# Performance work log

Measured on AMD Instinct MI355X. Metric: run time of the kernel, lower is better.

## Reference

```python
import jax, jax.numpy as jnp
import numpy as np

B, N, H = 4, 256, 128
EPS_BN = 1e-5     # nn.BatchNorm default eps
EPS_AGG = 1e-20   # NodeFeatureLayer.epsilon


def _linear_params(key, fan_in, shape_w, shape_b):
    kw, kb = jax.random.split(key)
    bound = 1.0 / np.sqrt(fan_in)
    w = jax.random.uniform(kw, shape_w, minval=-bound, maxval=bound, dtype=jnp.float32)
    b = jax.random.uniform(kb, shape_b, minval=-bound, maxval=bound, dtype=jnp.float32)
    return w, b


def setup_inputs() -> dict:
    key = jax.random.key(0)
    ks = jax.random.split(key, 6)
    Ue_w, Ue_b = _linear_params(ks[2], H, (H, H), (H,))
    Ve_w, Ve_b = _linear_params(ks[3], H, (H, H), (H,))
    Un_w, Un_b = _linear_params(ks[4], H, (H, H), (H,))
    Vn_w, Vn_b = _linear_params(ks[5], H, (H, H), (H,))
    return {
        "x": jax.random.normal(ks[0], (B, N, H), dtype=jnp.float32),
        "e": jax.random.normal(ks[1], (B, N, N, H), dtype=jnp.float32),
        "Ue_w": Ue_w, "Ue_b": Ue_b,   # EdgeFeatureLayer.U
        "Ve_w": Ve_w, "Ve_b": Ve_b,   # EdgeFeatureLayer.V
        "Un_w": Un_w, "Un_b": Un_b,   # NodeFeatureLayer.U
        "Vn_w": Vn_w, "Vn_b": Vn_b,   # NodeFeatureLayer.V
        "bn_x_g": jnp.ones((H,), jnp.float32), "bn_x_b": jnp.zeros((H,), jnp.float32),
        "bn_e_g": jnp.ones((H,), jnp.float32), "bn_e_b": jnp.zeros((H,), jnp.float32),
    }


def _bn(t, gamma, beta, axes):
    # BatchNorm with track_running_stats=False: normalize per-channel (last dim)
    # over all other axes using batch statistics (biased variance).
    m = jnp.mean(t, axis=axes, keepdims=True)
    v = jnp.var(t, axis=axes, keepdims=True)
    return (t - m) * jax.lax.rsqrt(v + EPS_BN) * gamma + beta


def reference(x, e, Ue_w, Ue_b, Ve_w, Ve_b, Un_w, Un_b, Vn_w, Vn_b,
              bn_x_g, bn_x_b, bn_e_g, bn_e_b):
    # EdgeFeatureLayer: Ue + Vx_rows + Vx_cols  -> (B,N,N,H)
    Vx = x @ Ve_w.T + Ve_b                       # (B,N,H)
    e_feat = (e @ Ue_w.T + Ue_b
              + Vx[:, :, None, :]                # rows: unsqueeze(2)
              + Vx[:, None, :, :])               # cols: unsqueeze(1)
    gates = jax.nn.sigmoid(e_feat)               # (B,N,N,H)

    # NodeFeatureLayer: Ux + sum_j(gate_ij * Vx_j) / (eps + sum_j gate_ij)
    Vnx = x @ Vn_w.T + Vn_b                      # (B,N,H)
    num = jnp.einsum('bijh,bjh->bih', gates, Vnx)
    den = EPS_AGG + jnp.sum(gates, axis=2)       # (B,N,H)
    x_feat = x @ Un_w.T + Un_b + num / den

    # norm -> (no dropout) -> relu -> residual
    x_new = x + jax.nn.relu(_bn(x_feat, bn_x_g, bn_x_b, (0, 1)))
    e_new = e + jax.nn.relu(_bn(e_feat, bn_e_g, bn_e_b, (0, 1, 2)))
    return (x_new, e_new)
```

## Files before the change

### kernel.cpp

```cpp
#include <hip/hip_runtime.h>
#include <math.h>

typedef short bf16x8 __attribute__((ext_vector_type(8)));
typedef float f32x4 __attribute__((ext_vector_type(4)));

#define BB 4
#define NN 256
#define HH 128
#define ME_ (BB*NN*NN)

#define VX_OFF   0
#define UX_OFF   131072
#define VXN_OFF  262144
#define NUM_OFF  393216
#define DEN_OFF  655360
#define PSUM_OFF 917504
#define PSQ_OFF  1179648
#define XF_OFF   1441792
#define PSR_OFF  1572864
#define PSQR_OFF 1581056
#define PSX_OFF  1589248
#define PSXX_OFF 1597440
#define SCE_OFF  1605632
#define SHE_OFF  1605760
#define SCX_OFF  1605888
#define SHX_OFF  1606016
#define W16_OFF  1606144

__device__ inline short f2bf(float f) {
    unsigned u = __builtin_bit_cast(unsigned, f);
    u += 0x7FFFu + ((u >> 16) & 1u);
    return (short)(u >> 16);
}
__device__ inline float bfbits2f(unsigned hi) {
    return __builtin_bit_cast(float, hi);
}

__global__ __launch_bounds__(256) void k_prep(const float* __restrict__ W,
                                              unsigned short* __restrict__ W16)
{
    int i = blockIdx.x * 256 + threadIdx.x;
    W16[i] = (unsigned short)f2bf(W[i]);
}

__global__ __launch_bounds__(256) void k_linx(
    const float* __restrict__ x,
    const float* __restrict__ Ve_w, const float* __restrict__ Ve_b,
    const float* __restrict__ Vn_w, const float* __restrict__ Vn_b,
    const float* __restrict__ Un_w, const float* __restrict__ Un_b,
    float* ws)
{
    __shared__ float xs[8 * 128];
    int t = threadIdx.x;
    int rowbase = blockIdx.x * 8;

    const float4* xg = (const float4*)(x + (size_t)rowbase * 128);
    ((float4*)xs)[t] = xg[t];
    __syncthreads();

    int h = t & 127, rh = t >> 7;
    float accV[4], accN[4], accU[4];
    float bV = Ve_b[h], bN = Vn_b[h], bU = Un_b[h];
    #pragma unroll
    for (int q = 0; q < 4; ++q) { accV[q] = bV; accN[q] = bN; accU[q] = bU; }

    const float4* wV = (const float4*)(Ve_w + (size_t)h * 128);
    const float4* wN = (const float4*)(Vn_w + (size_t)h * 128);
    const float4* wU = (const float4*)(Un_w + (size_t)h * 128);

    #pragma unroll 4
    for (int k4 = 0; k4 < 32; ++k4) {
        float4 wv = wV[k4], wn = wN[k4], wu = wU[k4];
        #pragma unroll
        for (int q = 0; q < 4; ++q) {
            float4 xv = *(const float4*)&xs[(rh + 2 * q) * 128 + k4 * 4];
            accV[q] += xv.x*wv.x + xv.y*wv.y + xv.z*wv.z + xv.w*wv.w;
            accN[q] += xv.x*wn.x + xv.y*wn.y + xv.z*wn.z + xv.w*wn.w;
            accU[q] += xv.x*wu.x + xv.y*wu.y + xv.z*wu.z + xv.w*wu.w;
        }
    }
    unsigned* VXN = (unsigned*)(ws + VXN_OFF);
    #pragma unroll
    for (int q = 0; q < 4; ++q) {
        size_t idx = (size_t)(rowbase + rh + 2 * q) * 128 + h;
        ws[VX_OFF + idx] = accV[q];
        ws[UX_OFF + idx] = accU[q];
        VXN[idx] = ((unsigned)(unsigned short)f2bf(accV[q]))
                 | ((unsigned)(unsigned short)f2bf(accN[q]) << 16);
    }
}

__device__ inline void load_raw(const float* __restrict__ eb, int row, int g,
                                float4* raw)
{
    const float* rp = eb + (size_t)row * 128 + g * 8;
    #pragma unroll
    for (int kc = 0; kc < 4; ++kc) {
        raw[2*kc]   = *(const float4*)(rp + kc * 32);
        raw[2*kc+1] = *(const float4*)(rp + kc * 32 + 4);
    }
}
__device__ inline void cvt_frag(const float4* raw, bf16x8* afr)
{
    #pragma unroll
    for (int kc = 0; kc < 4; ++kc) {
        float4 f0 = raw[2*kc], f1 = raw[2*kc+1];
        bf16x8 a;
        a[0] = f2bf(f0.x); a[1] = f2bf(f0.y); a[2] = f2bf(f0.z); a[3] = f2bf(f0.w);
        a[4] = f2bf(f1.x); a[5] = f2bf(f1.y); a[6] = f2bf(f1.z); a[7] = f2bf(f1.w);
        afr[kc] = a;
    }
}
__device__ inline bf16x8 ldsW(const short* Wl, int h, int kc, int g, int swz)
{
    return *(const bf16x8*)((const char*)Wl + h * 256 + ((kc * 64 + g * 16) ^ swz));
}

__global__ __launch_bounds__(256) void k_edge_stats(
    const float* __restrict__ e,
    const unsigned short* __restrict__ W16,
    const float* __restrict__ Ue_b,
    float* __restrict__ ws)
{
    __shared__ short Wl[16384];
    __shared__ float red[2048];
    int t   = threadIdx.x;
    int bx  = blockIdx.x;
    int bi  = bx >> 1, jh = bx & 1;
    int b   = bi >> 8;
    int wid = t >> 6, l = t & 63;
    int hsub = l & 15, g = l >> 4;
    int swz = (hsub & 7) << 4;
    int jbase = jh * 128 + wid * 32;

    const unsigned* VXNb = (const unsigned*)(ws + VXN_OFF) + (size_t)b * 32768;
    const float* eb = e + (size_t)bi * 32768;

    float4 raw[8];
    load_raw(eb, jbase + hsub, g, raw);

    float biasv[8];
    #pragma unroll
    for (int ct = 0; ct < 8; ++ct) {
        int h = ct * 16 + hsub;
        biasv[ct] = Ue_b[h] + ws[VX_OFF + (size_t)bi * 128 + h];
    }

    const int4* Wg = (const int4*)W16;
    #pragma unroll
    for (int p = 0; p < 8; ++p) {
        int s = t + 256 * p;
        int r = s >> 4, c = s & 15;
        int addr = r * 256 + ((c * 16) ^ ((r & 7) << 4));
        *(int4*)((char*)Wl + addr) = Wg[s];
    }
    __syncthreads();

    float num[8] = {0,0,0,0,0,0,0,0}, den[8] = {0,0,0,0,0,0,0,0};
    float se[8]  = {0,0,0,0,0,0,0,0}, sq[8]  = {0,0,0,0,0,0,0,0};

    bf16x8 afr[4];

    #pragma unroll
    for (int rt = 0; rt < 2; ++rt) {
        int jb = jbase + rt * 16;
        cvt_frag(raw, afr);
        if (rt == 0) load_raw(eb, jbase + 16 + hsub, g, raw);

        unsigned pkall[32];
        #pragma unroll
        for (int ct = 0; ct < 8; ++ct)
            #pragma unroll
            for (int r = 0; r < 4; ++r)
                pkall[ct * 4 + r] =
                    VXNb[(size_t)(jb + g * 4 + r) * 128 + ct * 16 + hsub];

        #pragma unroll
        for (int ct = 0; ct < 8; ++ct) {
            int h = ct * 16 + hsub;

            f32x4 acc = {0.f, 0.f, 0.f, 0.f};
            #pragma unroll
            for (int kc = 0; kc < 4; ++kc)
                acc = __builtin_amdgcn_mfma_f32_16x16x32_bf16(
                          afr[kc], ldsW(Wl, h, kc, g, swz), acc, 0, 0, 0);

            float bih = biasv[ct];
            #pragma unroll
            for (int r = 0; r < 4; ++r) {
                unsigned pk = pkall[ct * 4 + r];
                float vx  = bfbits2f(pk << 16);
                float vnx = bfbits2f(pk & 0xFFFF0000u);
                float v = acc[r] + bih + vx;
                float gv = __builtin_amdgcn_rcpf(1.0f + __expf(-v));
                num[ct] += gv * vnx;
                den[ct] += gv;
                se[ct]  += v;
                sq[ct]  += v * v;
            }
        }
    }

    #pragma unroll
    for (int ct = 0; ct < 8; ++ct) {
        float n = num[ct], d = den[ct], s1 = se[ct], s2 = sq[ct];
        n  += __shfl_xor(n, 32);  n  += __shfl_xor(n, 16);
        d  += __shfl_xor(d, 32);  d  += __shfl_xor(d, 16);
        s1 += __shfl_xor(s1, 32); s1 += __shfl_xor(s1, 16);
        s2 += __shfl_xor(s2, 32); s2 += __shfl_xor(s2, 16);
        if (l < 16) {
            int h = ct * 16 + l;
            red[0 * 512 + wid * 128 + h] = n;
            red[1 * 512 + wid * 128 + h] = d;
            red[2 * 512 + wid * 128 + h] = s1;
            red[3 * 512 + wid * 128 + h] = s2;
        }
    }
    __syncthreads();
    if (t < 128) {
        int h = t;
        float sn = 0.f, sd = 0.f;
        #pragma unroll
        for (int w = 0; w < 4; ++w) {
            sn += red[0 * 512 + w * 128 + h];
            sd += red[1 * 512 + w * 128 + h];
        }
        ws[NUM_OFF + (size_t)bx * 128 + h] = sn;
        ws[DEN_OFF + (size_t)bx * 128 + h] = sd;
    } else {
        int h = t - 128;
        float s1 = 0.f, s2 = 0.f;
        #pragma unroll
        for (int w = 0; w < 4; ++w) {
            s1 += red[2 * 512 + w * 128 + h];
            s2 += red[3 * 512 + w * 128 + h];
        }
        ws[PSUM_OFF + (size_t)bx * 128 + h] = s1;
        ws[PSQ_OFF  + (size_t)bx * 128 + h] = s2;
    }
}

__global__ __launch_bounds__(256) void k_red(float* ws)
{
    __shared__ float sm[1024];
    int t = threadIdx.x, bid = blockIdx.x;
    int h = t & 127, p = t >> 7;

    float s1 = 0.f, s2 = 0.f;
    #pragma unroll
    for (int q = 0; q < 16; ++q) {
        size_t idx = (size_t)(bid * 32 + p * 16 + q) * 128 + h;
        s1 += ws[PSUM_OFF + idx];
        s2 += ws[PSQ_OFF + idx];
    }
    float sx = 0.f, sxx = 0.f;
    #pragma unroll
    for (int q = 0; q < 8; ++q) {
        int bi = bid * 16 + p * 8 + q;
        size_t i0 = (size_t)(2 * bi) * 128 + h, i1 = (size_t)(2 * bi + 1) * 128 + h;
        float nm = ws[NUM_OFF + i0] + ws[NUM_OFF + i1];
        float dn = 1e-20f + ws[DEN_OFF + i0] + ws[DEN_OFF + i1];
        float v = ws[UX_OFF + (size_t)bi * 128 + h] + nm / dn;
        ws[XF_OFF + (size_t)bi * 128 + h] = v;
        sx += v; sxx += v * v;
    }
    sm[0 * 256 + p * 128 + h] = s1;
    sm[1 * 256 + p * 128 + h] = s2;
    sm[2 * 256 + p * 128 + h] = sx;
    sm[3 * 256 + p * 128 + h] = sxx;
    __syncthreads();
    if (t < 128) {
        ws[PSR_OFF  + (size_t)bid * 128 + h] = sm[0*256 + h] + sm[0*256 + 128 + h];
        ws[PSQR_OFF + (size_t)bid * 128 + h] = sm[1*256 + h] + sm[1*256 + 128 + h];
    } else {
        ws[PSX_OFF  + (size_t)bid * 128 + h] = sm[2*256 + h] + sm[2*256 + 128 + h];
        ws[PSXX_OFF + (size_t)bid * 128 + h] = sm[3*256 + h] + sm[3*256 + 128 + h];
    }
}

__global__ __launch_bounds__(128) void k_fin(
    const float* __restrict__ bn_x_g, const float* __restrict__ bn_x_b,
    const float* __restrict__ bn_e_g, const float* __restrict__ bn_e_b,
    float* ws)
{
    int h = threadIdx.x;
    float s1 = 0.f, s2 = 0.f, sx = 0.f, sxx = 0.f;
    for (int r = 0; r < 64; ++r) {
        size_t idx = (size_t)r * 128 + h;
        s1 += ws[PSR_OFF + idx];
        s2 += ws[PSQR_OFF + idx];
        sx += ws[PSX_OFF + idx];
        sxx+= ws[PSXX_OFF + idx];
    }
    float me = s1 / (float)ME_;
    float ve = s2 / (float)ME_ - me * me;
    float sce = bn_e_g[h] * rsqrtf(ve + 1e-5f);
    ws[SCE_OFF + h] = sce;
    ws[SHE_OFF + h] = bn_e_b[h] - me * sce;
    float mx = sx / 1024.0f;
    float vx = sxx / 1024.0f - mx * mx;
    float scx = bn_x_g[h] * rsqrtf(vx + 1e-5f);
    ws[SCX_OFF + h] = scx;
    ws[SHX_OFF + h] = bn_x_b[h] - mx * scx;
}

__global__ __launch_bounds__(256) void k_xnew(
    const float* __restrict__ x, const float* __restrict__ ws,
    float* __restrict__ out_x)
{
    __shared__ float sc[128], sh[128];
    int t = threadIdx.x;
    if (t < 128) sc[t] = ws[SCX_OFF + t];
    else         sh[t - 128] = ws[SHX_OFF + t - 128];
    __syncthreads();

    int i4 = blockIdx.x * 256 + t;
    int hb = (i4 & 31) * 4;
    float4 scv = *(const float4*)&sc[hb];
    float4 shv = *(const float4*)&sh[hb];
    float4 xf = ((const float4*)(ws + XF_OFF))[i4];
    float4 xv = ((const float4*)x)[i4];
    float4 o;
    o.x = xv.x + fmaxf(xf.x * scv.x + shv.x, 0.0f);
    o.y = xv.y + fmaxf(xf.y * scv.y + shv.y, 0.0f);
    o.z = xv.z + fmaxf(xf.z * scv.z + shv.z, 0.0f);
    o.w = xv.w + fmaxf(xf.w * scv.w + shv.w, 0.0f);
    ((float4*)out_x)[i4] = o;
}

__global__ __launch_bounds__(256) void k_edge_apply(
    const float* __restrict__ e,
    const unsigned short* __restrict__ W16,
    const float* __restrict__ Ue_b,
    const float* __restrict__ ws,
    float* __restrict__ out_e)
{
    __shared__ short Wl[16384];
    int t   = threadIdx.x;
    int bx  = blockIdx.x;
    int bi  = bx >> 1, jh = bx & 1;
    int b   = bi >> 8;
    int wid = t >> 6, l = t & 63;
    int hsub = l & 15, g = l >> 4;
    int swz = (hsub & 7) << 4;
    int jbase = jh * 128 + wid * 32;

    const float* VXf  = ws + VX_OFF + (size_t)b * 32768;
    const float* eb   = e     + (size_t)bi * 32768;
    float*       oute = out_e + (size_t)bi * 32768;

    float4 raw[8];
    load_raw(eb, jbase + hsub, g, raw);

    float biasv[8], sceR[8], sheR[8];
    #pragma unroll
    for (int ct = 0; ct < 8; ++ct) {
        int h = ct * 16 + hsub;
        biasv[ct] = Ue_b[h] + ws[VX_OFF + (size_t)bi * 128 + h];
        sceR[ct]  = ws[SCE_OFF + h];
        sheR[ct]  = ws[SHE_OFF + h];
    }

    const int4* Wg = (const int4*)W16;
    #pragma unroll
    for (int p = 0; p < 8; ++p) {
        int s = t + 256 * p;
        int r = s >> 4, c = s & 15;
        int addr = r * 256 + ((c * 16) ^ ((r & 7) << 4));
        *(int4*)((char*)Wl + addr) = Wg[s];
    }
    __syncthreads();

    bf16x8 afr[4];

    #pragma unroll
    for (int rt = 0; rt < 2; ++rt) {
        int jb = jbase + rt * 16;
        cvt_frag(raw, afr);
        if (rt == 0) load_raw(eb, jbase + 16 + hsub, g, raw);

        #pragma unroll
        for (int ct = 0; ct < 8; ++ct) {
            int h = ct * 16 + hsub;

            float vx[4], er[4];
            #pragma unroll
            for (int r = 0; r < 4; ++r) {
                size_t idx = (size_t)(jb + g * 4 + r) * 128 + h;
                vx[r] = VXf[idx];
                er[r] = eb[idx];
            }

            f32x4 acc = {0.f, 0.f, 0.f, 0.f};
            #pragma unroll
            for (int kc = 0; kc < 4; ++kc)
                acc = __builtin_amdgcn_mfma_f32_16x16x32_bf16(
                          afr[kc], ldsW(Wl, h, kc, g, swz), acc, 0, 0, 0);

            float bih = biasv[ct], sc = sceR[ct], sh = sheR[ct];
            #pragma unroll
            for (int r = 0; r < 4; ++r) {
                int j = jb + g * 4 + r;
                float v = acc[r] + bih + vx[r];
                float f = v * sc + sh;
                oute[(size_t)j * 128 + h] = er[r] + fmaxf(f, 0.0f);
            }
        }
    }
}

extern "C" void kernel_launch(void* const* d_in, const int* in_sizes, int n_in,
                              void* d_out, int out_size, void* d_ws, size_t ws_size,
                              hipStream_t stream)
{
    const float* x      = (const float*)d_in[0];
    const float* e      = (const float*)d_in[1];
    const float* Ue_w   = (const float*)d_in[2];
    const float* Ue_b   = (const float*)d_in[3];
    const float* Ve_w   = (const float*)d_in[4];
    const float* Ve_b   = (const float*)d_in[5];
    const float* Un_w   = (const float*)d_in[6];
    const float* Un_b   = (const float*)d_in[7];
    const float* Vn_w   = (const float*)d_in[8];
    const float* Vn_b   = (const float*)d_in[9];
    const float* bn_x_g = (const float*)d_in[10];
    const float* bn_x_b = (const float*)d_in[11];
    const float* bn_e_g = (const float*)d_in[12];
    const float* bn_e_b = (const float*)d_in[13];

    float* out   = (float*)d_out;
    float* out_x = out;
    float* out_e = out + 131072;
    float* ws    = (float*)d_ws;
    unsigned short* W16 = (unsigned short*)(ws + W16_OFF);

    k_prep       <<<64, 256, 0, stream>>>(Ue_w, W16);
    k_linx       <<<128, 256, 0, stream>>>(x, Ve_w, Ve_b, Vn_w, Vn_b, Un_w, Un_b, ws);
    k_edge_stats <<<2048, 256, 0, stream>>>(e, W16, Ue_b, ws);
    k_red        <<<64, 256, 0, stream>>>(ws);
    k_fin        <<<1, 128, 0, stream>>>(bn_x_g, bn_x_b, bn_e_g, bn_e_b, ws);
    k_xnew       <<<128, 256, 0, stream>>>(x, ws, out_x);
    k_edge_apply <<<2048, 256, 0, stream>>>(e, W16, Ue_b, ws, out_e);
}
```

Before: 134.7 us.

## Process a full row per edge-stats block and simplify partial reduction

Each k_edge_stats block now handles all 256 columns of one (b,i) row instead of half, halving the grid to 1024 blocks. This amortizes the shared-memory weight staging and bias loads over twice the work and removes the two-half combine in k_red. The VXN loads are moved inside the per-column-tile loop to reduce register pressure from the 32-entry prefetch array. The trade-off is fewer blocks for latency hiding and possibly more exposed global-load latency for the VXN values.

```diff
diff --git a/kernel.cpp b/kernel.cpp
--- a/kernel.cpp
+++ b/kernel.cpp
@@ -125,13 +125,12 @@
     __shared__ short Wl[16384];
     __shared__ float red[2048];
     int t   = threadIdx.x;
-    int bx  = blockIdx.x;
-    int bi  = bx >> 1, jh = bx & 1;
+    int bi  = blockIdx.x;
     int b   = bi >> 8;
     int wid = t >> 6, l = t & 63;
     int hsub = l & 15, g = l >> 4;
     int swz = (hsub & 7) << 4;
-    int jbase = jh * 128 + wid * 32;
+    int jbase = wid * 64;
 
     const unsigned* VXNb = (const unsigned*)(ws + VXN_OFF) + (size_t)b * 32768;
     const float* eb = e + (size_t)bi * 32768;
@@ -162,23 +161,20 @@
     bf16x8 afr[4];
 
     #pragma unroll
-    for (int rt = 0; rt < 2; ++rt) {
+    for (int rt = 0; rt < 4; ++rt) {
         int jb = jbase + rt * 16;
         cvt_frag(raw, afr);
-        if (rt == 0) load_raw(eb, jbase + 16 + hsub, g, raw);
-
-        unsigned pkall[32];
-        #pragma unroll
-        for (int ct = 0; ct < 8; ++ct)
-            #pragma unroll
-            for (int r = 0; r < 4; ++r)
-                pkall[ct * 4 + r] =
-                    VXNb[(size_t)(jb + g * 4 + r) * 128 + ct * 16 + hsub];
+        if (rt < 3) load_raw(eb, jb + 16 + hsub, g, raw);
 
         #pragma unroll
         for (int ct = 0; ct < 8; ++ct) {
             int h = ct * 16 + hsub;
 
+            unsigned pk[4];
+            #pragma unroll
+            for (int r = 0; r < 4; ++r)
+                pk[r] = VXNb[(size_t)(jb + g * 4 + r) * 128 + h];
+
             f32x4 acc = {0.f, 0.f, 0.f, 0.f};
             #pragma unroll
             for (int kc = 0; kc < 4; ++kc)
@@ -188,9 +184,8 @@
             float bih = biasv[ct];
             #pragma unroll
             for (int r = 0; r < 4; ++r) {
-                unsigned pk = pkall[ct * 4 + r];
-                float vx  = bfbits2f(pk << 16);
-                float vnx = bfbits2f(pk & 0xFFFF0000u);
+                float vx  = bfbits2f(pk[r] << 16);
+                float vnx = bfbits2f(pk[r] & 0xFFFF0000u);
                 float v = acc[r] + bih + vx;
                 float gv = __builtin_amdgcn_rcpf(1.0f + __expf(-v));
                 num[ct] += gv * vnx;
@@ -225,8 +220,8 @@
             sn += red[0 * 512 + w * 128 + h];
             sd += red[1 * 512 + w * 128 + h];
         }
-        ws[NUM_OFF + (size_t)bx * 128 + h] = sn;
-        ws[DEN_OFF + (size_t)bx * 128 + h] = sd;
+        ws[NUM_OFF + (size_t)bi * 128 + h] = sn;
+        ws[DEN_OFF + (size_t)bi * 128 + h] = sd;
     } else {
         int h = t - 128;
         float s1 = 0.f, s2 = 0.f;
@@ -235,8 +230,8 @@
             s1 += red[2 * 512 + w * 128 + h];
             s2 += red[3 * 512 + w * 128 + h];
         }
-        ws[PSUM_OFF + (size_t)bx * 128 + h] = s1;
-        ws[PSQ_OFF  + (size_t)bx * 128 + h] = s2;
+        ws[PSUM_OFF + (size_t)bi * 128 + h] = s1;
+        ws[PSQ_OFF  + (size_t)bi * 128 + h] = s2;
     }
 }
 
@@ -246,22 +241,17 @@
     int t = threadIdx.x, bid = blockIdx.x;
     int h = t & 127, p = t >> 7;
 
-    float s1 = 0.f, s2 = 0.f;
-    #pragma unroll
-    for (int q = 0; q < 16; ++q) {
-        size_t idx = (size_t)(bid * 32 + p * 16 + q) * 128 + h;
+    float s1 = 0.f, s2 = 0.f, sx = 0.f, sxx = 0.f;
+    #pragma unroll
+    for (int q = 0; q < 8; ++q) {
+        int bi = bid * 16 + p * 8 + q;
+        size_t idx = (size_t)bi * 128 + h;
         s1 += ws[PSUM_OFF + idx];
         s2 += ws[PSQ_OFF + idx];
-    }
-    float sx = 0.f, sxx = 0.f;
-    #pragma unroll
-    for (int q = 0; q < 8; ++q) {
-        int bi = bid * 16 + p * 8 + q;
-        size_t i0 = (size_t)(2 * bi) * 128 + h, i1 = (size_t)(2 * bi + 1) * 128 + h;
-        float nm = ws[NUM_OFF + i0] + ws[NUM_OFF + i1];
-        float dn = 1e-20f + ws[DEN_OFF + i0] + ws[DEN_OFF + i1];
-        float v = ws[UX_OFF + (size_t)bi * 128 + h] + nm / dn;
-        ws[XF_OFF + (size_t)bi * 128 + h] = v;
+        float nm = ws[NUM_OFF + idx];
+        float dn = 1e-20f + ws[DEN_OFF + idx];
+        float v = ws[UX_OFF + idx] + nm / dn;
+        ws[XF_OFF + idx] = v;
         sx += v; sxx += v * v;
     }
     sm[0 * 256 + p * 128 + h] = s1;
@@ -436,7 +426,7 @@
 
     k_prep       <<<64, 256, 0, stream>>>(Ue_w, W16);
     k_linx       <<<128, 256, 0, stream>>>(x, Ve_w, Ve_b, Vn_w, Vn_b, Un_w, Un_b, ws);
-    k_edge_stats <<<2048, 256, 0, stream>>>(e, W16, Ue_b, ws);
+    k_edge_stats <<<1024, 256, 0, stream>>>(e, W16, Ue_b, ws);
     k_red        <<<64, 256, 0, stream>>>(ws);
     k_fin        <<<1, 128, 0, stream>>>(bn_x_g, bn_x_b, bn_e_g, bn_e_b, ws);
     k_xnew       <<<128, 256, 0, stream>>>(x, ws, out_x);
```

After: 144.5 us. 7.3% more time.
